# Kernel tuning notes

Hardware: AMD Instinct MI355X
Metric: run time of the kernel (lower is better)

The kernel has to match this reference:

```python
import jax, jax.numpy as jnp
import numpy as np

N_NODES = 50000
N_EDGES = 600000
N_GRAPHS = 1000
IN_DIM = 128   # atom_feat_dim
HID = 128      # emb_dim
NEG_SLOPE = 0.01


def setup_inputs() -> dict:
    key = jax.random.key(0)
    k = jax.random.split(key, 6)
    drug_x = jax.random.normal(k[0], (N_NODES, IN_DIM), dtype=jnp.float32)
    edge_index = jax.random.randint(k[1], (2, N_EDGES), 0, N_NODES, dtype=jnp.int32)
    batch = jnp.sort(jax.random.randint(k[2], (N_NODES,), 0, N_GRAPHS, dtype=jnp.int32))
    # GCNConv parameters (glorot-ish init for weights, zero bias, as in PyG)
    W1 = jax.random.normal(k[3], (IN_DIM, HID), dtype=jnp.float32) * (1.0 / np.sqrt(IN_DIM))
    b1 = jnp.zeros((HID,), dtype=jnp.float32)
    W2 = jax.random.normal(k[4], (HID, HID), dtype=jnp.float32) * (1.0 / np.sqrt(HID))
    b2 = jnp.zeros((HID,), dtype=jnp.float32)
    return {"drug_x": drug_x, "W1": W1, "b1": b1, "W2": W2, "b2": b2,
            "edge_index": edge_index, "batch": batch}


def _gcn_conv(x, W, b, src, dst, n_nodes):
    """PyG GCNConv: lin -> add self-loops -> deg^-1/2 sym norm -> scatter-add -> +bias."""
    h = x @ W  # [N, H]
    ones = jnp.ones(src.shape[0], dtype=h.dtype)
    # degree on the target side, +1 for the self-loop
    deg = jax.ops.segment_sum(ones, dst, num_segments=n_nodes) + 1.0
    dinv = jax.lax.rsqrt(deg)  # [N]
    coef = dinv[src] * dinv[dst]  # [E]
    agg = jax.ops.segment_sum(h[src] * coef[:, None], dst, num_segments=n_nodes)
    # self-loop contribution: dinv[i]*dinv[i]*h[i]
    agg = agg + h * (dinv * dinv)[:, None]
    return agg + b


def _leaky_relu(x):
    return jnp.where(x > 0, x, NEG_SLOPE * x)


def reference(drug_x, W1, b1, W2, b2, edge_index, batch):
    src, dst = edge_index[0], edge_index[1]
    n = drug_x.shape[0]
    h = _leaky_relu(_gcn_conv(drug_x, W1, b1, src, dst, n))  # dropout = identity (eval)
    h = _leaky_relu(_gcn_conv(h, W2, b2, src, dst, n))
    # global_mean_pool over graph ids
    sums = jax.ops.segment_sum(h, batch, num_segments=N_GRAPHS)
    counts = jax.ops.segment_sum(jnp.ones((n,), h.dtype), batch, num_segments=N_GRAPHS)
    return sums / jnp.maximum(counts, 1.0)[:, None]
```

## Files before the change

### kernel.cpp

```cpp
#include <hip/hip_runtime.h>

#define DIM 128
#define NEG_SLOPE 0.01f
#define ELLW 64
#define CPAD 16
#define LDA 136
#define SPLIT 4
#define WPAD 132

typedef short short8 __attribute__((ext_vector_type(8)));
typedef float f32x4 __attribute__((ext_vector_type(4)));

__device__ __forceinline__ unsigned short f2bf(float f) {
    unsigned u = __float_as_uint(f);
    u = u + 0x7FFFu + ((u >> 16) & 1u);
    return (unsigned short)(u >> 16);
}
__device__ __forceinline__ float bf2f(unsigned short s) {
    return __uint_as_float((unsigned)s << 16);
}

__global__ __launch_bounds__(256) void k_fillprep(const int* __restrict__ src,
                                                  const int* __restrict__ dst,
                                                  const int* __restrict__ batch,
                                                  int* __restrict__ cursorPad,
                                                  int* __restrict__ eSrc,
                                                  const float* __restrict__ W1,
                                                  const float* __restrict__ W2,
                                                  unsigned short* __restrict__ Wt1,
                                                  unsigned short* __restrict__ Wt2,
                                                  int* __restrict__ gOff,
                                                  int nE, int nN, int nG) {
    int i = blockIdx.x * 256 + threadIdx.x;
    if (i < nE) {
        int s = src[i], d = dst[i];
        int pos = atomicAdd(&cursorPad[d * CPAD], 1);
        if (pos < ELLW) eSrc[(size_t)d * ELLW + pos] = s;
    }
    if (i < nN) {
        int b1 = batch[i];
        int b0 = (i == 0) ? -1 : batch[i - 1];
        for (int g = b0 + 1; g <= b1; ++g) gOff[g] = i;
        if (i == nN - 1) {
            for (int g = b1 + 1; g <= nG; ++g) gOff[g] = nN;
        }
    }
    if (i < 32768) {
        const float* W = (i < 16384) ? W1 : W2;
        unsigned short* Wt = (i < 16384) ? Wt1 : Wt2;
        int j = i & 16383;
        int k = j >> 7, n = j & 127;
        Wt[n * 128 + k] = f2bf(W[k * 128 + n]);
    }
}

__global__ __launch_bounds__(256) void k_gemm(const float* __restrict__ X,
                                              const unsigned short* __restrict__ Wt,
                                              const int* __restrict__ cursorPad,
                                              unsigned short* __restrict__ Y, int nRows) {
    __shared__ unsigned short sA[64 * LDA];
    const int t = threadIdx.x;
    const int row0 = blockIdx.x * 64;

#pragma unroll
    for (int rep = 0; rep < 8; ++rep) {
        int idx = t + rep * 256;
        int r = idx >> 5, k4 = (idx & 31) * 4;
        int gr = row0 + r;
        float4 v = make_float4(0.f, 0.f, 0.f, 0.f);
        if (gr < nRows) v = *(const float4*)&X[(size_t)gr * 128 + k4];
        ushort4 p;
        p.x = f2bf(v.x); p.y = f2bf(v.y); p.z = f2bf(v.z); p.w = f2bf(v.w);
        *(ushort4*)&sA[r * LDA + k4] = p;
    }
    __syncthreads();

    const int wave = t >> 6, lane = t & 63;
    const int l15 = lane & 15;
    const int koff = (lane >> 4) * 8;
    const int arow = wave * 16 + l15;

    short8 a[4];
#pragma unroll
    for (int ks = 0; ks < 4; ++ks)
        a[ks] = *(const short8*)&sA[arow * LDA + ks * 32 + koff];

    f32x4 acc[8];
#pragma unroll
    for (int c = 0; c < 8; ++c) acc[c] = (f32x4){0.f, 0.f, 0.f, 0.f};
#pragma unroll
    for (int c = 0; c < 8; ++c) {
        const unsigned short* wp = Wt + (size_t)(c * 16 + l15) * 128 + koff;
#pragma unroll
        for (int ks = 0; ks < 4; ++ks) {
            short8 b = *(const short8*)(wp + ks * 32);
            acc[c] = __builtin_amdgcn_mfma_f32_16x16x32_bf16(a[ks], b, acc[c], 0, 0, 0);
        }
    }
    const int orow = row0 + wave * 16 + (lane >> 4) * 4;
#pragma unroll
    for (int r = 0; r < 4; ++r) {
        int gr = orow + r;
        if (gr < nRows) {
            float dv = rsqrtf((float)cursorPad[gr * CPAD] + 1.0f);
#pragma unroll
            for (int c = 0; c < 8; ++c)
                Y[(size_t)gr * 128 + c * 16 + l15] = f2bf(acc[c][r] * dv);
        }
    }
}

#define ACCUM(v)                                         \
    do {                                                 \
        acc[0] += bf2f((v).x & 0xFFFFu);                 \
        acc[1] += __uint_as_float((v).x & 0xFFFF0000u);  \
        acc[2] += bf2f((v).y & 0xFFFFu);                 \
        acc[3] += __uint_as_float((v).y & 0xFFFF0000u);  \
        acc[4] += bf2f((v).z & 0xFFFFu);                 \
        acc[5] += __uint_as_float((v).z & 0xFFFF0000u);  \
        acc[6] += bf2f((v).w & 0xFFFFu);                 \
        acc[7] += __uint_as_float((v).w & 0xFFFF0000u);  \
    } while (0)

#define ACCUMF(v, s)                                                      \
    do {                                                                  \
        acc[0] = fmaf(bf2f((v).x & 0xFFFFu), (s), acc[0]);                \
        acc[1] = fmaf(__uint_as_float((v).x & 0xFFFF0000u), (s), acc[1]); \
        acc[2] = fmaf(bf2f((v).y & 0xFFFFu), (s), acc[2]);                \
        acc[3] = fmaf(__uint_as_float((v).y & 0xFFFF0000u), (s), acc[3]); \
        acc[4] = fmaf(bf2f((v).z & 0xFFFFu), (s), acc[4]);                \
        acc[5] = fmaf(__uint_as_float((v).z & 0xFFFF0000u), (s), acc[5]); \
        acc[6] = fmaf(bf2f((v).w & 0xFFFFu), (s), acc[6]);                \
        acc[7] = fmaf(__uint_as_float((v).w & 0xFFFF0000u), (s), acc[7]); \
    } while (0)

__device__ __forceinline__ void gather_body(const uint4* __restrict__ h4,
                                            const int* __restrict__ cursorPad,
                                            const int* __restrict__ eSrc,
                                            const float* __restrict__ bias,
                                            int i, int l, float* acc, int nN) {
    const int beg = i * ELLW;

    int4 s0 = *(const int4*)&eSrc[beg];
    int4 s1 = *(const int4*)&eSrc[beg + 4];
    int4 s2 = *(const int4*)&eSrc[beg + 8];
    int4 s3 = *(const int4*)&eSrc[beg + 12];
    const int cnt = cursorPad[i * CPAD];
    const uint4 hv = h4[(size_t)i * 16 + l];

    int sidx[16];
    sidx[0]  = s0.x; sidx[1]  = s0.y; sidx[2]  = s0.z; sidx[3]  = s0.w;
    sidx[4]  = s1.x; sidx[5]  = s1.y; sidx[6]  = s1.z; sidx[7]  = s1.w;
    sidx[8]  = s2.x; sidx[9]  = s2.y; sidx[10] = s2.z; sidx[11] = s2.w;
    sidx[12] = s3.x; sidx[13] = s3.y; sidx[14] = s3.z; sidx[15] = s3.w;
#pragma unroll
    for (int j = 0; j < 16; ++j) {
        unsigned us = (unsigned)sidx[j];
        sidx[j] = (us < (unsigned)nN) ? sidx[j] : 0;
    }

    uint4 v[16];
#pragma unroll
    for (int j = 0; j < 16; ++j) v[j] = h4[(size_t)sidx[j] * 16 + l];

    const int deg = min(cnt, ELLW);
    const int end = beg + deg;
    const float di = rsqrtf((float)cnt + 1.0f);

    acc[0] = bf2f(hv.x & 0xFFFFu);
    acc[1] = __uint_as_float(hv.x & 0xFFFF0000u);
    acc[2] = bf2f(hv.y & 0xFFFFu);
    acc[3] = __uint_as_float(hv.y & 0xFFFF0000u);
    acc[4] = bf2f(hv.z & 0xFFFFu);
    acc[5] = __uint_as_float(hv.z & 0xFFFF0000u);
    acc[6] = bf2f(hv.w & 0xFFFFu);
    acc[7] = __uint_as_float(hv.w & 0xFFFF0000u);

#pragma unroll
    for (int j = 0; j < 16; ++j) {
        float sc = (j < deg) ? 1.0f : 0.0f;
        ACCUMF(v[j], sc);
    }

    int e = beg + 16;
    for (; e + 8 <= end; e += 8) {
        int4 t0 = *(const int4*)&eSrc[e];
        int4 t1 = *(const int4*)&eSrc[e + 4];
        uint4 w[8];
        w[0] = h4[(size_t)t0.x * 16 + l];
        w[1] = h4[(size_t)t0.y * 16 + l];
        w[2] = h4[(size_t)t0.z * 16 + l];
        w[3] = h4[(size_t)t0.w * 16 + l];
        w[4] = h4[(size_t)t1.x * 16 + l];
        w[5] = h4[(size_t)t1.y * 16 + l];
        w[6] = h4[(size_t)t1.z * 16 + l];
        w[7] = h4[(size_t)t1.w * 16 + l];
#pragma unroll
        for (int j = 0; j < 8; ++j) ACCUM(w[j]);
    }
    if (e + 4 <= end) {
        int4 t0 = *(const int4*)&eSrc[e];
        uint4 w[4];
        w[0] = h4[(size_t)t0.x * 16 + l];
        w[1] = h4[(size_t)t0.y * 16 + l];
        w[2] = h4[(size_t)t0.z * 16 + l];
        w[3] = h4[(size_t)t0.w * 16 + l];
#pragma unroll
        for (int j = 0; j < 4; ++j) ACCUM(w[j]);
        e += 4;
    }
    if (e + 2 <= end) {
        int t0 = eSrc[e], t1 = eSrc[e + 1];
        uint4 w0 = h4[(size_t)t0 * 16 + l];
        uint4 w1 = h4[(size_t)t1 * 16 + l];
        ACCUM(w0);
        ACCUM(w1);
        e += 2;
    }
    if (e < end) {
        int t0 = eSrc[e];
        uint4 w0 = h4[(size_t)t0 * 16 + l];
        ACCUM(w0);
    }

    float4 b0 = *(const float4*)&bias[l * 8];
    float4 b1 = *(const float4*)&bias[l * 8 + 4];
    acc[0] = acc[0] * di + b0.x; acc[0] = acc[0] > 0.f ? acc[0] : NEG_SLOPE * acc[0];
    acc[1] = acc[1] * di + b0.y; acc[1] = acc[1] > 0.f ? acc[1] : NEG_SLOPE * acc[1];
    acc[2] = acc[2] * di + b0.z; acc[2] = acc[2] > 0.f ? acc[2] : NEG_SLOPE * acc[2];
    acc[3] = acc[3] * di + b0.w; acc[3] = acc[3] > 0.f ? acc[3] : NEG_SLOPE * acc[3];
    acc[4] = acc[4] * di + b1.x; acc[4] = acc[4] > 0.f ? acc[4] : NEG_SLOPE * acc[4];
    acc[5] = acc[5] * di + b1.y; acc[5] = acc[5] > 0.f ? acc[5] : NEG_SLOPE * acc[5];
    acc[6] = acc[6] * di + b1.z; acc[6] = acc[6] > 0.f ? acc[6] : NEG_SLOPE * acc[6];
    acc[7] = acc[7] * di + b1.w; acc[7] = acc[7] > 0.f ? acc[7] : NEG_SLOPE * acc[7];
}
#undef ACCUM
#undef ACCUMF

__global__ __launch_bounds__(256) void k_gg(const uint4* __restrict__ h4in,
                                            const int* __restrict__ cursorPad,
                                            const int* __restrict__ eSrc,
                                            const float* __restrict__ bias,
                                            const unsigned short* __restrict__ Wt,
                                            unsigned short* __restrict__ Y, int nN) {
    __shared__ unsigned short sA[16 * LDA];
    const int t = threadIdx.x;
    const int row0 = blockIdx.x * 16;
    const int lg = t >> 4;
    const int l = t & 15;

    {
        int i = row0 + lg;
        float acc[8];
        if (i < nN) {
            gather_body(h4in, cursorPad, eSrc, bias, i, l, acc, nN);
        } else {
#pragma unroll
            for (int j = 0; j < 8; ++j) acc[j] = 0.0f;
        }
        ushort4 p0, p1;
        p0.x = f2bf(acc[0]); p0.y = f2bf(acc[1]); p0.z = f2bf(acc[2]); p0.w = f2bf(acc[3]);
        p1.x = f2bf(acc[4]); p1.y = f2bf(acc[5]); p1.z = f2bf(acc[6]); p1.w = f2bf(acc[7]);
        *(ushort4*)&sA[lg * LDA + l * 8] = p0;
        *(ushort4*)&sA[lg * LDA + l * 8 + 4] = p1;
    }
    __syncthreads();

    const int wave = t >> 6, lane = t & 63;
    const int l15 = lane & 15;
    const int koff = (lane >> 4) * 8;

    short8 a[4];
#pragma unroll
    for (int ks = 0; ks < 4; ++ks)
        a[ks] = *(const short8*)&sA[l15 * LDA + ks * 32 + koff];

    f32x4 acc[2];
#pragma unroll
    for (int cb = 0; cb < 2; ++cb) acc[cb] = (f32x4){0.f, 0.f, 0.f, 0.f};
#pragma unroll
    for (int cb = 0; cb < 2; ++cb) {
        const int c = wave * 2 + cb;
        const unsigned short* wp = Wt + (size_t)(c * 16 + l15) * 128 + koff;
#pragma unroll
        for (int ks = 0; ks < 4; ++ks) {
            short8 b = *(const short8*)(wp + ks * 32);
            acc[cb] = __builtin_amdgcn_mfma_f32_16x16x32_bf16(a[ks], b, acc[cb], 0, 0, 0);
        }
    }
    const int orow = row0 + (lane >> 4) * 4;
#pragma unroll
    for (int r = 0; r < 4; ++r) {
        int gr = orow + r;
        if (gr < nN) {
            float dv = rsqrtf((float)cursorPad[gr * CPAD] + 1.0f);
#pragma unroll
            for (int cb = 0; cb < 2; ++cb)
                Y[(size_t)gr * 128 + (wave * 2 + cb) * 16 + l15] = f2bf(acc[cb][r] * dv);
        }
    }
}

__global__ __launch_bounds__(256) void k_gp(const uint4* __restrict__ h4in,
                                            const int* __restrict__ cursorPad,
                                            const int* __restrict__ eSrc,
                                            const float* __restrict__ bias,
                                            const int* __restrict__ gOff,
                                            float* __restrict__ out, int nN, int nG) {
    __shared__ float accW[4 * WPAD];
    const int g = blockIdx.x / SPLIT;
    const int part = blockIdx.x % SPLIT;
    const int t = threadIdx.x;
    const int beg = gOff[g], end = gOff[g + 1];
    const int lg = t >> 4, l = t & 15;
    const int wave = t >> 6, lane = t & 63;

    float acc8[8];
#pragma unroll
    for (int j = 0; j < 8; ++j) acc8[j] = 0.0f;

    for (int base = beg + part * 16; base < end; base += SPLIT * 16) {
        int i = base + lg;
        if (i < end) {
            float a[8];
            gather_body(h4in, cursorPad, eSrc, bias, i, l, a, nN);
#pragma unroll
            for (int j = 0; j < 8; ++j) acc8[j] += a[j];
        }
    }
#pragma unroll
    for (int j = 0; j < 8; ++j) {
        acc8[j] += __shfl_down(acc8[j], 32);
        acc8[j] += __shfl_down(acc8[j], 16);
    }
    if (lane < 16) {
        *(float4*)&accW[wave * WPAD + lane * 8] =
            make_float4(acc8[0], acc8[1], acc8[2], acc8[3]);
        *(float4*)&accW[wave * WPAD + lane * 8 + 4] =
            make_float4(acc8[4], acc8[5], acc8[6], acc8[7]);
    }
    __syncthreads();
    if (t < 128) {
        float s = accW[0 * WPAD + t] + accW[1 * WPAD + t] +
                  accW[2 * WPAD + t] + accW[3 * WPAD + t];
        float cnt = (float)(end - beg);
        atomicAdd(&out[(size_t)g * DIM + t], s / fmaxf(cnt, 1.0f));
    }
}

extern "C" void kernel_launch(void* const* d_in, const int* in_sizes, int n_in,
                              void* d_out, int out_size, void* d_ws, size_t ws_size,
                              hipStream_t stream) {
    const float* X  = (const float*)d_in[0];
    const float* W1 = (const float*)d_in[1];
    const float* b1 = (const float*)d_in[2];
    const float* W2 = (const float*)d_in[3];
    const float* b2 = (const float*)d_in[4];
    const int*   ei = (const int*)d_in[5];
    const int*   batch = (const int*)d_in[6];
    float* out = (float*)d_out;

    const int NN = in_sizes[0] / DIM;
    const int NE = in_sizes[5] / 2;
    const int NG = out_size / DIM;

    const int* src = ei;
    const int* dst = ei + NE;

    char* ws = (char*)d_ws;
    size_t o = 0;
    auto alloc = [&](size_t bytes) {
        char* p = ws + o;
        o += (bytes + 1023) & ~(size_t)1023;
        return p;
    };
    int* cursorPad = (int*)alloc((size_t)NN * CPAD * 4);
    int* gOff      = (int*)alloc((size_t)(NG + 1) * 4);
    unsigned short* Wt1 = (unsigned short*)alloc((size_t)16384 * 2);
    unsigned short* Wt2 = (unsigned short*)alloc((size_t)16384 * 2);
    int*   eSrc    = (int*)alloc((size_t)NN * ELLW * 4);
    unsigned short* bufA = (unsigned short*)alloc((size_t)NN * DIM * 2);
    unsigned short* bufB = (unsigned short*)alloc((size_t)NN * DIM * 2);

    hipMemsetAsync(cursorPad, 0, (size_t)NN * CPAD * 4, stream);
    hipMemsetAsync(out, 0, (size_t)out_size * 4, stream);

    const int B = 256;

    k_fillprep<<<(NE + B - 1) / B, B, 0, stream>>>(src, dst, batch, cursorPad, eSrc,
                                                   W1, W2, Wt1, Wt2, gOff, NE, NN, NG);

    k_gemm<<<(NN + 63) / 64, B, 0, stream>>>(X, Wt1, cursorPad, bufA, NN);

    k_gg<<<(NN + 15) / 16, B, 0, stream>>>((const uint4*)bufA, cursorPad, eSrc, b1,
                                           Wt2, bufB, NN);

    k_gp<<<NG * SPLIT, B, 0, stream>>>((const uint4*)bufB, cursorPad, eSrc, b2,
                                       gOff, out, NN, NG);
}
```

Before: 196.3 us.

## Chunk features into 32-column slabs and pack neighbor lists with 16-bit indices

Stores intermediate bf16 features in four column-chunked slabs so each gather block touches a smaller working set that fits in cache better. Packs the degree and the first 30 neighbor indices as 16-bit values into one 64-byte metadata row per node, with overflow going to a 16-bit ELL array. The fused gather+GEMM kernel is split into separate gather and GEMM2 kernels, and pooling now writes its output directly instead of using atomics. Nontemporal loads and stores are added throughout. The 16-bit indices only work while the node count stays below 65536, and unused index slots are read as zero-filled entries, which relies on the memset.

Result: slower. 225.4 us (+14.8%).

```diff
diff --git a/kernel.cpp b/kernel.cpp
--- a/kernel.cpp
+++ b/kernel.cpp
@@ -2,14 +2,16 @@
 
 #define DIM 128
 #define NEG_SLOPE 0.01f
+#define NCHUNK 4
+#define CH 32
 #define ELLW 64
-#define CPAD 16
+#define MIDX 30
 #define LDA 136
-#define SPLIT 4
-#define WPAD 132
 
 typedef short short8 __attribute__((ext_vector_type(8)));
 typedef float f32x4 __attribute__((ext_vector_type(4)));
+typedef unsigned int u32x4 __attribute__((ext_vector_type(4)));
+typedef unsigned short ushort_t;
 
 __device__ __forceinline__ unsigned short f2bf(float f) {
     unsigned u = __float_as_uint(f);
@@ -23,8 +25,9 @@
 __global__ __launch_bounds__(256) void k_fillprep(const int* __restrict__ src,
                                                   const int* __restrict__ dst,
                                                   const int* __restrict__ batch,
-                                                  int* __restrict__ cursorPad,
-                                                  int* __restrict__ eSrc,
+                                                  unsigned int* __restrict__ metaU,
+                                                  unsigned short* __restrict__ metaH,
+                                                  unsigned short* __restrict__ eSrcU,
                                                   const float* __restrict__ W1,
                                                   const float* __restrict__ W2,
                                                   unsigned short* __restrict__ Wt1,
@@ -34,8 +37,9 @@
     int i = blockIdx.x * 256 + threadIdx.x;
     if (i < nE) {
         int s = src[i], d = dst[i];
-        int pos = atomicAdd(&cursorPad[d * CPAD], 1);
-        if (pos < ELLW) eSrc[(size_t)d * ELLW + pos] = s;
+        int pos = atomicAdd((int*)&metaU[(size_t)d * 16], 1);
+        if (pos < MIDX) metaH[(size_t)d * 32 + 2 + pos] = (unsigned short)s;
+        else if (pos < ELLW) eSrcU[(size_t)d * ELLW + pos] = (unsigned short)s;
     }
     if (i < nN) {
         int b1 = batch[i];
@@ -51,62 +55,6 @@
         int j = i & 16383;
         int k = j >> 7, n = j & 127;
         Wt[n * 128 + k] = f2bf(W[k * 128 + n]);
-    }
-}
-
-__global__ __launch_bounds__(256) void k_gemm(const float* __restrict__ X,
-                                              const unsigned short* __restrict__ Wt,
-                                              const int* __restrict__ cursorPad,
-                                              unsigned short* __restrict__ Y, int nRows) {
-    __shared__ unsigned short sA[64 * LDA];
-    const int t = threadIdx.x;
-    const int row0 = blockIdx.x * 64;
-
-#pragma unroll
-    for (int rep = 0; rep < 8; ++rep) {
-        int idx = t + rep * 256;
-        int r = idx >> 5, k4 = (idx & 31) * 4;
-        int gr = row0 + r;
-        float4 v = make_float4(0.f, 0.f, 0.f, 0.f);
-        if (gr < nRows) v = *(const float4*)&X[(size_t)gr * 128 + k4];
-        ushort4 p;
-        p.x = f2bf(v.x); p.y = f2bf(v.y); p.z = f2bf(v.z); p.w = f2bf(v.w);
-        *(ushort4*)&sA[r * LDA + k4] = p;
-    }
-    __syncthreads();
-
-    const int wave = t >> 6, lane = t & 63;
-    const int l15 = lane & 15;
-    const int koff = (lane >> 4) * 8;
-    const int arow = wave * 16 + l15;
-
-    short8 a[4];
-#pragma unroll
-    for (int ks = 0; ks < 4; ++ks)
-        a[ks] = *(const short8*)&sA[arow * LDA + ks * 32 + koff];
-
-    f32x4 acc[8];
-#pragma unroll
-    for (int c = 0; c < 8; ++c) acc[c] = (f32x4){0.f, 0.f, 0.f, 0.f};
-#pragma unroll
-    for (int c = 0; c < 8; ++c) {
-        const unsigned short* wp = Wt + (size_t)(c * 16 + l15) * 128 + koff;
-#pragma unroll
-        for (int ks = 0; ks < 4; ++ks) {
-            short8 b = *(const short8*)(wp + ks * 32);
-            acc[c] = __builtin_amdgcn_mfma_f32_16x16x32_bf16(a[ks], b, acc[c], 0, 0, 0);
-        }
-    }
-    const int orow = row0 + wave * 16 + (lane >> 4) * 4;
-#pragma unroll
-    for (int r = 0; r < 4; ++r) {
-        int gr = orow + r;
-        if (gr < nRows) {
-            float dv = rsqrtf((float)cursorPad[gr * CPAD] + 1.0f);
-#pragma unroll
-            for (int c = 0; c < 8; ++c)
-                Y[(size_t)gr * 128 + c * 16 + l15] = f2bf(acc[c][r] * dv);
-        }
     }
 }
 
@@ -127,6 +75,18 @@
         acc[0] = fmaf(bf2f((v).x & 0xFFFFu), (s), acc[0]);                \
         acc[1] = fmaf(__uint_as_float((v).x & 0xFFFF0000u), (s), acc[1]); \
         acc[2] = fmaf(bf2f((v).y & 0xFFFFu), (s), acc[2]);                \
+        acc[3] = fmaf(bf2f((v).y >> 16 << 16 == 0 ? 0 : (unsigned short)((v).y >> 16)) * 0.f + __uint_as_float((v).y & 0xFFFF0000u), (s), acc[3]); \
+        acc[4] = fmaf(bf2f((v).z & 0xFFFFu), (s), acc[4]);                \
+        acc[5] = fmaf(__uint_as_float((v).z & 0xFFFF0000u), (s), acc[5]); \
+        acc[6] = fmaf(bf2f((v).w & 0xFFFFu), (s), acc[6]);                \
+        acc[7] = fmaf(__uint_as_float((v).w & 0xFFFF0000u), (s), acc[7]); \
+    } while (0)
+#undef ACCUMF
+#define ACCUMF(v, s)                                                      \
+    do {                                                                  \
+        acc[0] = fmaf(bf2f((v).x & 0xFFFFu), (s), acc[0]);                \
+        acc[1] = fmaf(__uint_as_float((v).x & 0xFFFF0000u), (s), acc[1]); \
+        acc[2] = fmaf(bf2f((v).y & 0xFFFFu), (s), acc[2]);                \
         acc[3] = fmaf(__uint_as_float((v).y & 0xFFFF0000u), (s), acc[3]); \
         acc[4] = fmaf(bf2f((v).z & 0xFFFFu), (s), acc[4]);                \
         acc[5] = fmaf(__uint_as_float((v).z & 0xFFFF0000u), (s), acc[5]); \
@@ -134,37 +94,41 @@
         acc[7] = fmaf(__uint_as_float((v).w & 0xFFFF0000u), (s), acc[7]); \
     } while (0)
 
-__device__ __forceinline__ void gather_body(const uint4* __restrict__ h4,
-                                            const int* __restrict__ cursorPad,
-                                            const int* __restrict__ eSrc,
-                                            const float* __restrict__ bias,
-                                            int i, int l, float* acc, int nN) {
-    const int beg = i * ELLW;
-
-    int4 s0 = *(const int4*)&eSrc[beg];
-    int4 s1 = *(const int4*)&eSrc[beg + 4];
-    int4 s2 = *(const int4*)&eSrc[beg + 8];
-    int4 s3 = *(const int4*)&eSrc[beg + 12];
-    const int cnt = cursorPad[i * CPAD];
-    const uint4 hv = h4[(size_t)i * 16 + l];
-
-    int sidx[16];
-    sidx[0]  = s0.x; sidx[1]  = s0.y; sidx[2]  = s0.z; sidx[3]  = s0.w;
-    sidx[4]  = s1.x; sidx[5]  = s1.y; sidx[6]  = s1.z; sidx[7]  = s1.w;
-    sidx[8]  = s2.x; sidx[9]  = s2.y; sidx[10] = s2.z; sidx[11] = s2.w;
-    sidx[12] = s3.x; sidx[13] = s3.y; sidx[14] = s3.z; sidx[15] = s3.w;
-#pragma unroll
-    for (int j = 0; j < 16; ++j) {
-        unsigned us = (unsigned)sidx[j];
-        sidx[j] = (us < (unsigned)nN) ? sidx[j] : 0;
-    }
-
-    uint4 v[16];
-#pragma unroll
-    for (int j = 0; j < 16; ++j) v[j] = h4[(size_t)sidx[j] * 16 + l];
+__device__ __forceinline__ void gather_chunk(const u32x4* __restrict__ hb,
+                                             const u32x4* __restrict__ meta4,
+                                             const unsigned short* __restrict__ eSrcU,
+                                             const float* __restrict__ bias,
+                                             int i, int l, float* acc) {
+    const u32x4* mrow = meta4 + (size_t)i * 4;
+    u32x4 m0 = __builtin_nontemporal_load(mrow + 0);
+    u32x4 m1 = __builtin_nontemporal_load(mrow + 1);
+    u32x4 m2 = __builtin_nontemporal_load(mrow + 2);
+    u32x4 m3 = __builtin_nontemporal_load(mrow + 3);
+    u32x4 hv = hb[(size_t)i * 4 + l];
+
+    const int cnt = (int)m0.x;
+    int idx[30];
+    idx[0]  = m0.y & 0xFFFFu;  idx[1]  = m0.y >> 16;
+    idx[2]  = m0.z & 0xFFFFu;  idx[3]  = m0.z >> 16;
+    idx[4]  = m0.w & 0xFFFFu;  idx[5]  = m0.w >> 16;
+    idx[6]  = m1.x & 0xFFFFu;  idx[7]  = m1.x >> 16;
+    idx[8]  = m1.y & 0xFFFFu;  idx[9]  = m1.y >> 16;
+    idx[10] = m1.z & 0xFFFFu;  idx[11] = m1.z >> 16;
+    idx[12] = m1.w & 0xFFFFu;  idx[13] = m1.w >> 16;
+    idx[14] = m2.x & 0xFFFFu;  idx[15] = m2.x >> 16;
+    idx[16] = m2.y & 0xFFFFu;  idx[17] = m2.y >> 16;
+    idx[18] = m2.z & 0xFFFFu;  idx[19] = m2.z >> 16;
+    idx[20] = m2.w & 0xFFFFu;  idx[21] = m2.w >> 16;
+    idx[22] = m3.x & 0xFFFFu;  idx[23] = m3.x >> 16;
+    idx[24] = m3.y & 0xFFFFu;  idx[25] = m3.y >> 16;
+    idx[26] = m3.z & 0xFFFFu;  idx[27] = m3.z >> 16;
+    idx[28] = m3.w & 0xFFFFu;  idx[29] = m3.w >> 16;
+
+    u32x4 v[16];
+#pragma unroll
+    for (int j = 0; j < 16; ++j) v[j] = hb[(size_t)idx[j] * 4 + l];
 
     const int deg = min(cnt, ELLW);
-    const int end = beg + deg;
     const float di = rsqrtf((float)cnt + 1.0f);
 
     acc[0] = bf2f(hv.x & 0xFFFFu);
@@ -182,45 +146,23 @@
         ACCUMF(v[j], sc);
     }
 
-    int e = beg + 16;
-    for (; e + 8 <= end; e += 8) {
-        int4 t0 = *(const int4*)&eSrc[e];
-        int4 t1 = *(const int4*)&eSrc[e + 4];
-        uint4 w[8];
-        w[0] = h4[(size_t)t0.x * 16 + l];
-        w[1] = h4[(size_t)t0.y * 16 + l];
-        w[2] = h4[(size_t)t0.z * 16 + l];
-        w[3] = h4[(size_t)t0.w * 16 + l];
-        w[4] = h4[(size_t)t1.x * 16 + l];
-        w[5] = h4[(size_t)t1.y * 16 + l];
-        w[6] = h4[(size_t)t1.z * 16 + l];
-        w[7] = h4[(size_t)t1.w * 16 + l];
-#pragma unroll
-        for (int j = 0; j < 8; ++j) ACCUM(w[j]);
-    }
-    if (e + 4 <= end) {
-        int4 t0 = *(const int4*)&eSrc[e];
-        uint4 w[4];
-        w[0] = h4[(size_t)t0.x * 16 + l];
-        w[1] = h4[(size_t)t0.y * 16 + l];
-        w[2] = h4[(size_t)t0.z * 16 + l];
-        w[3] = h4[(size_t)t0.w * 16 + l];
-#pragma unroll
-        for (int j = 0; j < 4; ++j) ACCUM(w[j]);
-        e += 4;
-    }
-    if (e + 2 <= end) {
-        int t0 = eSrc[e], t1 = eSrc[e + 1];
-        uint4 w0 = h4[(size_t)t0 * 16 + l];
-        uint4 w1 = h4[(size_t)t1 * 16 + l];
-        ACCUM(w0);
-        ACCUM(w1);
-        e += 2;
-    }
-    if (e < end) {
-        int t0 = eSrc[e];
-        uint4 w0 = h4[(size_t)t0 * 16 + l];
-        ACCUM(w0);
+    if (deg > 16) {
+        u32x4 w[14];
+#pragma unroll
+        for (int j = 0; j < 14; ++j) w[j] = hb[(size_t)idx[16 + j] * 4 + l];
+#pragma unroll
+        for (int j = 0; j < 14; ++j) {
+            float sc = (16 + j < deg) ? 1.0f : 0.0f;
+            ACCUMF(w[j], sc);
+        }
+    }
+
+    if (deg > MIDX) {
+        for (int e = MIDX; e < deg; ++e) {
+            int s = (int)__builtin_nontemporal_load(&eSrcU[(size_t)i * ELLW + e]);
+            u32x4 w0 = hb[(size_t)s * 4 + l];
+            ACCUM(w0);
+        }
     }
 
     float4 b0 = *(const float4*)&bias[l * 8];
@@ -234,96 +176,177 @@
     acc[6] = acc[6] * di + b1.z; acc[6] = acc[6] > 0.f ? acc[6] : NEG_SLOPE * acc[6];
     acc[7] = acc[7] * di + b1.w; acc[7] = acc[7] > 0.f ? acc[7] : NEG_SLOPE * acc[7];
 }
-#undef ACCUM
-#undef ACCUMF
-
-__global__ __launch_bounds__(256) void k_gg(const uint4* __restrict__ h4in,
-                                            const int* __restrict__ cursorPad,
-                                            const int* __restrict__ eSrc,
-                                            const float* __restrict__ bias,
-                                            const unsigned short* __restrict__ Wt,
-                                            unsigned short* __restrict__ Y, int nN) {
-    __shared__ unsigned short sA[16 * LDA];
+
+__global__ __launch_bounds__(256) void k_gemm1(const float* __restrict__ X,
+                                               const unsigned short* __restrict__ Wt,
+                                               const unsigned int* __restrict__ metaU,
+                                               unsigned short* __restrict__ Y, int nRows) {
+    __shared__ unsigned short sA[64 * LDA];
     const int t = threadIdx.x;
-    const int row0 = blockIdx.x * 16;
-    const int lg = t >> 4;
-    const int l = t & 15;
-
-    {
-        int i = row0 + lg;
-        float acc[8];
-        if (i < nN) {
-            gather_body(h4in, cursorPad, eSrc, bias, i, l, acc, nN);
-        } else {
-#pragma unroll
-            for (int j = 0; j < 8; ++j) acc[j] = 0.0f;
-        }
-        ushort4 p0, p1;
-        p0.x = f2bf(acc[0]); p0.y = f2bf(acc[1]); p0.z = f2bf(acc[2]); p0.w = f2bf(acc[3]);
-        p1.x = f2bf(acc[4]); p1.y = f2bf(acc[5]); p1.z = f2bf(acc[6]); p1.w = f2bf(acc[7]);
-        *(ushort4*)&sA[lg * LDA + l * 8] = p0;
-        *(ushort4*)&sA[lg * LDA + l * 8 + 4] = p1;
+    const int row0 = blockIdx.x * 64;
+
+#pragma unroll
+    for (int rep = 0; rep < 8; ++rep) {
+        int idx = t + rep * 256;
+        int r = idx >> 5, k4 = (idx & 31) * 4;
+        int gr = row0 + r;
+        f32x4 v = (f32x4){0.f, 0.f, 0.f, 0.f};
+        if (gr < nRows) v = __builtin_nontemporal_load((const f32x4*)&X[(size_t)gr * 128 + k4]);
+        ushort4 p;
+        p.x = f2bf(v.x); p.y = f2bf(v.y); p.z = f2bf(v.z); p.w = f2bf(v.w);
+        *(ushort4*)&sA[r * LDA + k4] = p;
     }
     __syncthreads();
 
     const int wave = t >> 6, lane = t & 63;
     const int l15 = lane & 15;
     const int koff = (lane >> 4) * 8;
+    const int arow = wave * 16 + l15;
 
     short8 a[4];
 #pragma unroll
     for (int ks = 0; ks < 4; ++ks)
-        a[ks] = *(const short8*)&sA[l15 * LDA + ks * 32 + koff];
-
-    f32x4 acc[2];
-#pragma unroll
-    for (int cb = 0; cb < 2; ++cb) acc[cb] = (f32x4){0.f, 0.f, 0.f, 0.f};
-#pragma unroll
-    for (int cb = 0; cb < 2; ++cb) {
-        const int c = wave * 2 + cb;
+        a[ks] = *(const short8*)&sA[arow * LDA + ks * 32 + koff];
+
+    f32x4 acc[8];
+#pragma unroll
+    for (int c = 0; c < 8; ++c) acc[c] = (f32x4){0.f, 0.f, 0.f, 0.f};
+#pragma unroll
+    for (int c = 0; c < 8; ++c) {
         const unsigned short* wp = Wt + (size_t)(c * 16 + l15) * 128 + koff;
 #pragma unroll
         for (int ks = 0; ks < 4; ++ks) {
             short8 b = *(const short8*)(wp + ks * 32);
-            acc[cb] = __builtin_amdgcn_mfma_f32_16x16x32_bf16(a[ks], b, acc[cb], 0, 0, 0);
-        }
-    }
-    const int orow = row0 + (lane >> 4) * 4;
+            acc[c] = __builtin_amdgcn_mfma_f32_16x16x32_bf16(a[ks], b, acc[c], 0, 0, 0);
+        }
+    }
+    const int orow = row0 + wave * 16 + (lane >> 4) * 4;
 #pragma unroll
     for (int r = 0; r < 4; ++r) {
         int gr = orow + r;
-        if (gr < nN) {
-            float dv = rsqrtf((float)cursorPad[gr * CPAD] + 1.0f);
-#pragma unroll
-            for (int cb = 0; cb < 2; ++cb)
-                Y[(size_t)gr * 128 + (wave * 2 + cb) * 16 + l15] = f2bf(acc[cb][r] * dv);
-        }
-    }
-}
-
-__global__ __launch_bounds__(256) void k_gp(const uint4* __restrict__ h4in,
-                                            const int* __restrict__ cursorPad,
-                                            const int* __restrict__ eSrc,
+        if (gr < nRows) {
+            int cnt = (int)__builtin_nontemporal_load(&metaU[(size_t)gr * 16]);
+            float dv = rsqrtf((float)cnt + 1.0f);
+#pragma unroll
+            for (int c = 0; c < 8; ++c) {
+                size_t addr = ((size_t)((c >> 1) * nRows) + gr) * CH + (c & 1) * 16 + l15;
+                __builtin_nontemporal_store(f2bf(acc[c][r] * dv), &Y[addr]);
+            }
+        }
+    }
+}
+
+__global__ __launch_bounds__(256) void k_gemm2(const unsigned short* __restrict__ Xb,
+                                               const unsigned short* __restrict__ Wt,
+                                               const unsigned int* __restrict__ metaU,
+                                               unsigned short* __restrict__ Y, int nRows) {
+    __shared__ unsigned short sA[64 * LDA];
+    const int t = threadIdx.x;
+    const int row0 = blockIdx.x * 64;
+
+#pragma unroll
+    for (int rep = 0; rep < 4; ++rep) {
+        int idx = t + rep * 256;
+        int r = idx >> 4, s = idx & 15;
+        int c = s >> 2, q = s & 3;
+        int gr = row0 + r;
+        u32x4 v = (u32x4){0u, 0u, 0u, 0u};
+        if (gr < nRows)
+            v = __builtin_nontemporal_load(
+                (const u32x4*)&Xb[((size_t)(c * nRows) + gr) * CH + q * 8]);
+        *(u32x4*)&sA[r * LDA + s * 8] = v;
+    }
+    __syncthreads();
+
+    const int wave = t >> 6, lane = t & 63;
+    const int l15 = lane & 15;
+    const int koff = (lane >> 4) * 8;
+    const int arow = wave * 16 + l15;
+
+    short8 a[4];
+#pragma unroll
+    for (int ks = 0; ks < 4; ++ks)
+        a[ks] = *(const short8*)&sA[arow * LDA + ks * 32 + koff];
+
+    f32x4 acc[8];
+#pragma unroll
+    for (int c = 0; c < 8; ++c) acc[c] = (f32x4){0.f, 0.f, 0.f, 0.f};
+#pragma unroll
+    for (int c = 0; c < 8; ++c) {
+        const unsigned short* wp = Wt + (size_t)(c * 16 + l15) * 128 + koff;
+#pragma unroll
+        for (int ks = 0; ks < 4; ++ks) {
+            short8 b = *(const short8*)(wp + ks * 32);
+            acc[c] = __builtin_amdgcn_mfma_f32_16x16x32_bf16(a[ks], b, acc[c], 0, 0, 0);
+        }
+    }
+    const int orow = row0 + wave * 16 + (lane >> 4) * 4;
+#pragma unroll
+    for (int r = 0; r < 4; ++r) {
+        int gr = orow + r;
+        if (gr < nRows) {
+            int cnt = (int)__builtin_nontemporal_load(&metaU[(size_t)gr * 16]);
+            float dv = rsqrtf((float)cnt + 1.0f);
+#pragma unroll
+            for (int c = 0; c < 8; ++c) {
+                size_t addr = ((size_t)((c >> 1) * nRows) + gr) * CH + (c & 1) * 16 + l15;
+                __builtin_nontemporal_store(f2bf(acc[c][r] * dv), &Y[addr]);
+            }
+        }
+    }
+}
+
+__global__ __launch_bounds__(256) void k_gather1(const u32x4* __restrict__ hbase,
+                                                 const u32x4* __restrict__ meta4,
+                                                 const unsigned short* __restrict__ eSrcU,
+                                                 const float* __restrict__ bias,
+                                                 unsigned short* __restrict__ outB,
+                                                 int nN) {
+    const int tile = blockIdx.x >> 2;
+    const int c = blockIdx.x & 3;
+    const int t = threadIdx.x;
+    const int i = tile * 64 + (t >> 2);
+    const int l = t & 3;
+    if (i >= nN) return;
+
+    const u32x4* hb = hbase + (size_t)c * nN * 4;
+    float acc[8];
+    gather_chunk(hb, meta4, eSrcU, bias + c * CH, i, l, acc);
+
+    u32x4 p;
+    p.x = (unsigned)f2bf(acc[0]) | ((unsigned)f2bf(acc[1]) << 16);
+    p.y = (unsigned)f2bf(acc[2]) | ((unsigned)f2bf(acc[3]) << 16);
+    p.z = (unsigned)f2bf(acc[4]) | ((unsigned)f2bf(acc[5]) << 16);
+    p.w = (unsigned)f2bf(acc[6]) | ((unsigned)f2bf(acc[7]) << 16);
+    __builtin_nontemporal_store(
+        p, (u32x4*)&outB[((size_t)(c * nN) + i) * CH + l * 8]);
+}
+
+__global__ __launch_bounds__(256) void k_gp(const u32x4* __restrict__ hbase,
+                                            const u32x4* __restrict__ meta4,
+                                            const unsigned short* __restrict__ eSrcU,
                                             const float* __restrict__ bias,
                                             const int* __restrict__ gOff,
-                                            float* __restrict__ out, int nN, int nG) {
-    __shared__ float accW[4 * WPAD];
-    const int g = blockIdx.x / SPLIT;
-    const int part = blockIdx.x % SPLIT;
+                                            float* __restrict__ out, int nN) {
+    __shared__ float red[4 * 32];
+    const int g = blockIdx.x >> 2;
+    const int c = blockIdx.x & 3;
     const int t = threadIdx.x;
     const int beg = gOff[g], end = gOff[g + 1];
-    const int lg = t >> 4, l = t & 15;
+    const int ln = t >> 2, l = t & 3;
     const int wave = t >> 6, lane = t & 63;
 
+    const u32x4* hb = hbase + (size_t)c * nN * 4;
+
     float acc8[8];
 #pragma unroll
     for (int j = 0; j < 8; ++j) acc8[j] = 0.0f;
 
-    for (int base = beg + part * 16; base < end; base += SPLIT * 16) {
-        int i = base + lg;
+    for (int i0 = beg; i0 < end; i0 += 64) {
+        int i = i0 + ln;
         if (i < end) {
             float a[8];
-            gather_body(h4in, cursorPad, eSrc, bias, i, l, a, nN);
+            gather_chunk(hb, meta4, eSrcU, bias + c * CH, i, l, a);
 #pragma unroll
             for (int j = 0; j < 8; ++j) acc8[j] += a[j];
         }
@@ -332,19 +355,18 @@
     for (int j = 0; j < 8; ++j) {
         acc8[j] += __shfl_down(acc8[j], 32);
         acc8[j] += __shfl_down(acc8[j], 16);
-    }
-    if (lane < 16) {
-        *(float4*)&accW[wave * WPAD + lane * 8] =
-            make_float4(acc8[0], acc8[1], acc8[2], acc8[3]);
-        *(float4*)&accW[wave * WPAD + lane * 8 + 4] =
-            make_float4(acc8[4], acc8[5], acc8[6], acc8[7]);
+        acc8[j] += __shfl_down(acc8[j], 8);
+        acc8[j] += __shfl_down(acc8[j], 4);
+    }
+    if (lane < 4) {
+#pragma unroll
+        for (int j = 0; j < 8; ++j) red[wave * 32 + lane * 8 + j] = acc8[j];
     }
     __syncthreads();
-    if (t < 128) {
-        float s = accW[0 * WPAD + t] + accW[1 * WPAD + t] +
-                  accW[2 * WPAD + t] + accW[3 * WPAD + t];
-        float cnt = (float)(end - beg);
-        atomicAdd(&out[(size_t)g * DIM + t], s / fmaxf(cnt, 1.0f));
+    if (t < 32) {
+        float s = red[t] + red[32 + t] + red[64 + t] + red[96 + t];
+        float n = (float)(end - beg);
+        out[(size_t)g * DIM + c * CH + t] = s / fmaxf(n, 1.0f);
     }
 }
 
@@ -374,27 +396,31 @@
         o += (bytes + 1023) & ~(size_t)1023;
         return p;
     };
-    int* cursorPad = (int*)alloc((size_t)NN * CPAD * 4);
-    int* gOff      = (int*)alloc((size_t)(NG + 1) * 4);
+    unsigned int* meta = (unsigned int*)alloc((size_t)NN * 64);
+    int* gOff          = (int*)alloc((size_t)(NG + 1) * 4);
     unsigned short* Wt1 = (unsigned short*)alloc((size_t)16384 * 2);
     unsigned short* Wt2 = (unsigned short*)alloc((size_t)16384 * 2);
-    int*   eSrc    = (int*)alloc((size_t)NN * ELLW * 4);
+    unsigned short* eSrcU = (unsigned short*)alloc((size_t)NN * ELLW * 2);
     unsigned short* bufA = (unsigned short*)alloc((size_t)NN * DIM * 2);
     unsigned short* bufB = (unsigned short*)alloc((size_t)NN * DIM * 2);
-
-    hipMemsetAsync(cursorPad, 0, (size_t)NN * CPAD * 4, stream);
-    hipMemsetAsync(out, 0, (size_t)out_size * 4, stream);
+    unsigned short* bufC = (unsigned short*)alloc((size_t)NN * DIM * 2);
+
+    hipMemsetAsync(meta, 0, (size_t)NN * 64, stream);
 
     const int B = 256;
-
-    k_fillprep<<<(NE + B - 1) / B, B, 0, stream>>>(src, dst, batch, cursorPad, eSrc,
+    const int nT = (NN + 63) / 64;
+
+    k_fillprep<<<(NE + B - 1) / B, B, 0, stream>>>(src, dst, batch, meta,
+                                                   (unsigned short*)meta, eSrcU,
                                                    W1, W2, Wt1, Wt2, gOff, NE, NN, NG);
 
-    k_gemm<<<(NN + 63) / 64, B, 0, stream>>>(X, Wt1, cursorPad, bufA, NN);
-
-    k_gg<<<(NN + 15) / 16, B, 0, stream>>>((const uint4*)bufA, cursorPad, eSrc, b1,
-                                           Wt2, bufB, NN);
-
-    k_gp<<<NG * SPLIT, B, 0, stream>>>((const uint4*)bufB, cursorPad, eSrc, b2,
-                                       gOff, out, NN, NG);
-}
+    k_gemm1<<<nT, B, 0, stream>>>(X, Wt1, meta, bufA, NN);
+
+    k_gather1<<<nT * NCHUNK, B, 0, stream>>>((const u32x4*)bufA, (const u32x4*)meta,
+                                             eSrcU, b1, bufB, NN);
+
+    k_gemm2<<<nT, B, 0, stream>>>(bufB, Wt2, meta, bufC, NN);
+
+    k_gp<<<NG * NCHUNK, B, 0, stream>>>((const u32x4*)bufC, (const u32x4*)meta,
+                                        eSrcU, b2, gOff, out, NN);
+}
```

## Pack degree and 16-bit neighbor indices into one 64-byte row per node

Applied to the files above, without the earlier changes.

Replaces the padded cursor array and the 64-wide int32 ELL table with a compact per-node 64-byte metadata row holding the count plus 30 uint16 source indices, and a uint16 spill area for neighbors 31 to 64. The gather then reads the count and first 30 indices in four uint4 loads, and the memset and index traffic shrink. Nontemporal loads and stores are added on the edge, X and output streams. This relies on node ids fitting in 16 bits, which holds only for N=50000, and it drops the bounds clamp on indices.

New measurement: 206.0 us. 1.05x slower.

```diff
diff --git a/kernel.cpp b/kernel.cpp
--- a/kernel.cpp
+++ b/kernel.cpp
@@ -2,8 +2,9 @@
 
 #define DIM 128
 #define NEG_SLOPE 0.01f
-#define ELLW 64
-#define CPAD 16
+#define MIDX 30
+#define SPILLW 34
+#define CAP 64
 #define LDA 136
 #define SPLIT 4
 #define WPAD 132
@@ -23,8 +24,9 @@
 __global__ __launch_bounds__(256) void k_fillprep(const int* __restrict__ src,
                                                   const int* __restrict__ dst,
                                                   const int* __restrict__ batch,
-                                                  int* __restrict__ cursorPad,
-                                                  int* __restrict__ eSrc,
+                                                  unsigned int* __restrict__ metaU,
+                                                  unsigned short* __restrict__ metaH,
+                                                  unsigned short* __restrict__ spill,
                                                   const float* __restrict__ W1,
                                                   const float* __restrict__ W2,
                                                   unsigned short* __restrict__ Wt1,
@@ -33,9 +35,11 @@
                                                   int nE, int nN, int nG) {
     int i = blockIdx.x * 256 + threadIdx.x;
     if (i < nE) {
-        int s = src[i], d = dst[i];
-        int pos = atomicAdd(&cursorPad[d * CPAD], 1);
-        if (pos < ELLW) eSrc[(size_t)d * ELLW + pos] = s;
+        int s = __builtin_nontemporal_load(&src[i]);
+        int d = __builtin_nontemporal_load(&dst[i]);
+        int pos = atomicAdd((int*)&metaU[(size_t)d * 16], 1);
+        if (pos < MIDX) metaH[(size_t)d * 32 + 2 + pos] = (unsigned short)s;
+        else if (pos < CAP) spill[(size_t)d * SPILLW + (pos - MIDX)] = (unsigned short)s;
     }
     if (i < nN) {
         int b1 = batch[i];
@@ -51,62 +55,6 @@
         int j = i & 16383;
         int k = j >> 7, n = j & 127;
         Wt[n * 128 + k] = f2bf(W[k * 128 + n]);
-    }
-}
-
-__global__ __launch_bounds__(256) void k_gemm(const float* __restrict__ X,
-                                              const unsigned short* __restrict__ Wt,
-                                              const int* __restrict__ cursorPad,
-                                              unsigned short* __restrict__ Y, int nRows) {
-    __shared__ unsigned short sA[64 * LDA];
-    const int t = threadIdx.x;
-    const int row0 = blockIdx.x * 64;
-
-#pragma unroll
-    for (int rep = 0; rep < 8; ++rep) {
-        int idx = t + rep * 256;
-        int r = idx >> 5, k4 = (idx & 31) * 4;
-        int gr = row0 + r;
-        float4 v = make_float4(0.f, 0.f, 0.f, 0.f);
-        if (gr < nRows) v = *(const float4*)&X[(size_t)gr * 128 + k4];
-        ushort4 p;
-        p.x = f2bf(v.x); p.y = f2bf(v.y); p.z = f2bf(v.z); p.w = f2bf(v.w);
-        *(ushort4*)&sA[r * LDA + k4] = p;
-    }
-    __syncthreads();
-
-    const int wave = t >> 6, lane = t & 63;
-    const int l15 = lane & 15;
-    const int koff = (lane >> 4) * 8;
-    const int arow = wave * 16 + l15;
-
-    short8 a[4];
-#pragma unroll
-    for (int ks = 0; ks < 4; ++ks)
-        a[ks] = *(const short8*)&sA[arow * LDA + ks * 32 + koff];
-
-    f32x4 acc[8];
-#pragma unroll
-    for (int c = 0; c < 8; ++c) acc[c] = (f32x4){0.f, 0.f, 0.f, 0.f};
-#pragma unroll
-    for (int c = 0; c < 8; ++c) {
-        const unsigned short* wp = Wt + (size_t)(c * 16 + l15) * 128 + koff;
-#pragma unroll
-        for (int ks = 0; ks < 4; ++ks) {
-            short8 b = *(const short8*)(wp + ks * 32);
-            acc[c] = __builtin_amdgcn_mfma_f32_16x16x32_bf16(a[ks], b, acc[c], 0, 0, 0);
-        }
-    }
-    const int orow = row0 + wave * 16 + (lane >> 4) * 4;
-#pragma unroll
-    for (int r = 0; r < 4; ++r) {
-        int gr = orow + r;
-        if (gr < nRows) {
-            float dv = rsqrtf((float)cursorPad[gr * CPAD] + 1.0f);
-#pragma unroll
-            for (int c = 0; c < 8; ++c)
-                Y[(size_t)gr * 128 + c * 16 + l15] = f2bf(acc[c][r] * dv);
-        }
     }
 }
 
@@ -135,37 +83,34 @@
     } while (0)
 
 __device__ __forceinline__ void gather_body(const uint4* __restrict__ h4,
-                                            const int* __restrict__ cursorPad,
-                                            const int* __restrict__ eSrc,
+                                            const uint4* __restrict__ meta4,
+                                            const unsigned short* __restrict__ spill,
                                             const float* __restrict__ bias,
-                                            int i, int l, float* acc, int nN) {
-    const int beg = i * ELLW;
-
-    int4 s0 = *(const int4*)&eSrc[beg];
-    int4 s1 = *(const int4*)&eSrc[beg + 4];
-    int4 s2 = *(const int4*)&eSrc[beg + 8];
-    int4 s3 = *(const int4*)&eSrc[beg + 12];
-    const int cnt = cursorPad[i * CPAD];
+                                            int i, int l, float* acc) {
+    const uint4* mrow = meta4 + (size_t)i * 4;
+    uint4 m0 = mrow[0];
+    uint4 m1 = mrow[1];
+    uint4 m2 = mrow[2];
+    uint4 m3 = mrow[3];
     const uint4 hv = h4[(size_t)i * 16 + l];
 
-    int sidx[16];
-    sidx[0]  = s0.x; sidx[1]  = s0.y; sidx[2]  = s0.z; sidx[3]  = s0.w;
-    sidx[4]  = s1.x; sidx[5]  = s1.y; sidx[6]  = s1.z; sidx[7]  = s1.w;
-    sidx[8]  = s2.x; sidx[9]  = s2.y; sidx[10] = s2.z; sidx[11] = s2.w;
-    sidx[12] = s3.x; sidx[13] = s3.y; sidx[14] = s3.z; sidx[15] = s3.w;
-#pragma unroll
-    for (int j = 0; j < 16; ++j) {
-        unsigned us = (unsigned)sidx[j];
-        sidx[j] = (us < (unsigned)nN) ? sidx[j] : 0;
-    }
+    const int cnt = (int)m0.x;
+    const int deg = min(cnt, CAP);
+    const float di = rsqrtf((float)cnt + 1.0f);
+
+    int idx[16];
+    idx[0]  = m0.y & 0xFFFFu;  idx[1]  = m0.y >> 16;
+    idx[2]  = m0.z & 0xFFFFu;  idx[3]  = m0.z >> 16;
+    idx[4]  = m0.w & 0xFFFFu;  idx[5]  = m0.w >> 16;
+    idx[6]  = m1.x & 0xFFFFu;  idx[7]  = m1.x >> 16;
+    idx[8]  = m1.y & 0xFFFFu;  idx[9]  = m1.y >> 16;
+    idx[10] = m1.z & 0xFFFFu;  idx[11] = m1.z >> 16;
+    idx[12] = m1.w & 0xFFFFu;  idx[13] = m1.w >> 16;
+    idx[14] = m2.x & 0xFFFFu;  idx[15] = m2.x >> 16;
 
     uint4 v[16];
 #pragma unroll
-    for (int j = 0; j < 16; ++j) v[j] = h4[(size_t)sidx[j] * 16 + l];
-
-    const int deg = min(cnt, ELLW);
-    const int end = beg + deg;
-    const float di = rsqrtf((float)cnt + 1.0f);
+    for (int j = 0; j < 16; ++j) v[j] = h4[(size_t)idx[j] * 16 + l];
 
     acc[0] = bf2f(hv.x & 0xFFFFu);
     acc[1] = __uint_as_float(hv.x & 0xFFFF0000u);
@@ -182,45 +127,31 @@
         ACCUMF(v[j], sc);
     }
 
-    int e = beg + 16;
-    for (; e + 8 <= end; e += 8) {
-        int4 t0 = *(const int4*)&eSrc[e];
-        int4 t1 = *(const int4*)&eSrc[e + 4];
-        uint4 w[8];
-        w[0] = h4[(size_t)t0.x * 16 + l];
-        w[1] = h4[(size_t)t0.y * 16 + l];
-        w[2] = h4[(size_t)t0.z * 16 + l];
-        w[3] = h4[(size_t)t0.w * 16 + l];
-        w[4] = h4[(size_t)t1.x * 16 + l];
-        w[5] = h4[(size_t)t1.y * 16 + l];
-        w[6] = h4[(size_t)t1.z * 16 + l];
-        w[7] = h4[(size_t)t1.w * 16 + l];
-#pragma unroll
-        for (int j = 0; j < 8; ++j) ACCUM(w[j]);
-    }
-    if (e + 4 <= end) {
-        int4 t0 = *(const int4*)&eSrc[e];
-        uint4 w[4];
-        w[0] = h4[(size_t)t0.x * 16 + l];
-        w[1] = h4[(size_t)t0.y * 16 + l];
-        w[2] = h4[(size_t)t0.z * 16 + l];
-        w[3] = h4[(size_t)t0.w * 16 + l];
-#pragma unroll
-        for (int j = 0; j < 4; ++j) ACCUM(w[j]);
-        e += 4;
-    }
-    if (e + 2 <= end) {
-        int t0 = eSrc[e], t1 = eSrc[e + 1];
-        uint4 w0 = h4[(size_t)t0 * 16 + l];
-        uint4 w1 = h4[(size_t)t1 * 16 + l];
-        ACCUM(w0);
-        ACCUM(w1);
-        e += 2;
-    }
-    if (e < end) {
-        int t0 = eSrc[e];
-        uint4 w0 = h4[(size_t)t0 * 16 + l];
-        ACCUM(w0);
+    if (deg > 16) {
+        int idx2[14];
+        idx2[0]  = m2.y & 0xFFFFu;  idx2[1]  = m2.y >> 16;
+        idx2[2]  = m2.z & 0xFFFFu;  idx2[3]  = m2.z >> 16;
+        idx2[4]  = m2.w & 0xFFFFu;  idx2[5]  = m2.w >> 16;
+        idx2[6]  = m3.x & 0xFFFFu;  idx2[7]  = m3.x >> 16;
+        idx2[8]  = m3.y & 0xFFFFu;  idx2[9]  = m3.y >> 16;
+        idx2[10] = m3.z & 0xFFFFu;  idx2[11] = m3.z >> 16;
+        idx2[12] = m3.w & 0xFFFFu;  idx2[13] = m3.w >> 16;
+        uint4 w[14];
+#pragma unroll
+        for (int j = 0; j < 14; ++j) w[j] = h4[(size_t)idx2[j] * 16 + l];
+#pragma unroll
+        for (int j = 0; j < 14; ++j) {
+            float sc = (16 + j < deg) ? 1.0f : 0.0f;
+            ACCUMF(w[j], sc);
+        }
+    }
+
+    if (deg > MIDX) {
+        for (int e = MIDX; e < deg; ++e) {
+            int s = (int)spill[(size_t)i * SPILLW + (e - MIDX)];
+            uint4 w0 = h4[(size_t)s * 16 + l];
+            ACCUM(w0);
+        }
     }
 
     float4 b0 = *(const float4*)&bias[l * 8];
@@ -234,12 +165,70 @@
     acc[6] = acc[6] * di + b1.z; acc[6] = acc[6] > 0.f ? acc[6] : NEG_SLOPE * acc[6];
     acc[7] = acc[7] * di + b1.w; acc[7] = acc[7] > 0.f ? acc[7] : NEG_SLOPE * acc[7];
 }
-#undef ACCUM
-#undef ACCUMF
+
+__global__ __launch_bounds__(256) void k_gemm(const float* __restrict__ X,
+                                              const unsigned short* __restrict__ Wt,
+                                              const unsigned int* __restrict__ metaU,
+                                              unsigned short* __restrict__ Y, int nRows) {
+    __shared__ unsigned short sA[64 * LDA];
+    const int t = threadIdx.x;
+    const int row0 = blockIdx.x * 64;
+
+#pragma unroll
+    for (int rep = 0; rep < 8; ++rep) {
+        int idx = t + rep * 256;
+        int r = idx >> 5, k4 = (idx & 31) * 4;
+        int gr = row0 + r;
+        f32x4 v = (f32x4){0.f, 0.f, 0.f, 0.f};
+        if (gr < nRows)
+            v = __builtin_nontemporal_load((const f32x4*)&X[(size_t)gr * 128 + k4]);
+        ushort4 p;
+        p.x = f2bf(v.x); p.y = f2bf(v.y); p.z = f2bf(v.z); p.w = f2bf(v.w);
+        *(ushort4*)&sA[r * LDA + k4] = p;
+    }
+    __syncthreads();
+
+    const int wave = t >> 6, lane = t & 63;
+    const int l15 = lane & 15;
+    const int koff = (lane >> 4) * 8;
+    const int arow = wave * 16 + l15;
+
+    short8 a[4];
+#pragma unroll
+    for (int ks = 0; ks < 4; ++ks)
+        a[ks] = *(const short8*)&sA[arow * LDA + ks * 32 + koff];
+
+    f32x4 acc[8];
+#pragma unroll
+    for (int c = 0; c < 8; ++c) acc[c] = (f32x4){0.f, 0.f, 0.f, 0.f};
+#pragma unroll
+    for (int c = 0; c < 8; ++c) {
+        const unsigned short* wp = Wt + (size_t)(c * 16 + l15) * 128 + koff;
+#pragma unroll
+        for (int ks = 0; ks < 4; ++ks) {
+            short8 b = *(const short8*)(wp + ks * 32);
+            acc[c] = __builtin_amdgcn_mfma_f32_16x16x32_bf16(a[ks], b, acc[c], 0, 0, 0);
+        }
+    }
+    const int orow = row0 + wave * 16 + (lane >> 4) * 4;
+#pragma unroll
+    for (int r = 0; r < 4; ++r) {
+        int gr = orow + r;
+        if (gr < nRows) {
+            int cnt = (int)metaU[(size_t)gr * 16];
+            float dv = rsqrtf((float)cnt + 1.0f);
+#pragma unroll
+            for (int c = 0; c < 8; ++c)
+                __builtin_nontemporal_store(f2bf(acc[c][r] * dv),
+                                            &Y[(size_t)gr * 128 + c * 16 + l15]);
+        }
+    }
+}
 
 __global__ __launch_bounds__(256) void k_gg(const uint4* __restrict__ h4in,
-                                            const int* __restrict__ cursorPad,
-                                            const int* __restrict__ eSrc,
+                                            const uint4* __restrict__ meta4,
+                                            const unsigned int* __restrict__ metaU,
+                                            const unsigned short* __restrict__ spill,
                                             const float* __restrict__ bias,
                                             const unsigned short* __restrict__ Wt,
                                             unsigned short* __restrict__ Y, int nN) {
@@ -253,7 +242,7 @@
         int i = row0 + lg;
         float acc[8];
         if (i < nN) {
-            gather_body(h4in, cursorPad, eSrc, bias, i, l, acc, nN);
+            gather_body(h4in, meta4, spill, bias, i, l, acc);
         } else {
 #pragma unroll
             for (int j = 0; j < 8; ++j) acc[j] = 0.0f;
@@ -293,17 +282,20 @@
     for (int r = 0; r < 4; ++r) {
         int gr = orow + r;
         if (gr < nN) {
-            float dv = rsqrtf((float)cursorPad[gr * CPAD] + 1.0f);
+            int cnt = (int)metaU[(size_t)gr * 16];
+            float dv = rsqrtf((float)cnt + 1.0f);
 #pragma unroll
             for (int cb = 0; cb < 2; ++cb)
-                Y[(size_t)gr * 128 + (wave * 2 + cb) * 16 + l15] = f2bf(acc[cb][r] * dv);
+                __builtin_nontemporal_store(
+                    f2bf(acc[cb][r] * dv),
+                    &Y[(size_t)gr * 128 + (wave * 2 + cb) * 16 + l15]);
         }
     }
 }
 
 __global__ __launch_bounds__(256) void k_gp(const uint4* __restrict__ h4in,
-                                            const int* __restrict__ cursorPad,
-                                            const int* __restrict__ eSrc,
+                                            const uint4* __restrict__ meta4,
+                                            const unsigned short* __restrict__ spill,
                                             const float* __restrict__ bias,
                                             const int* __restrict__ gOff,
                                             float* __restrict__ out, int nN, int nG) {
@@ -323,7 +315,7 @@
         int i = base + lg;
         if (i < end) {
             float a[8];
-            gather_body(h4in, cursorPad, eSrc, bias, i, l, a, nN);
+            gather_body(h4in, meta4, spill, bias, i, l, a);
 #pragma unroll
             for (int j = 0; j < 8; ++j) acc8[j] += a[j];
         }
@@ -374,27 +366,28 @@
         o += (bytes + 1023) & ~(size_t)1023;
         return p;
     };
-    int* cursorPad = (int*)alloc((size_t)NN * CPAD * 4);
-    int* gOff      = (int*)alloc((size_t)(NG + 1) * 4);
+    unsigned int* meta = (unsigned int*)alloc((size_t)NN * 64);
+    int* gOff          = (int*)alloc((size_t)(NG + 1) * 4);
     unsigned short* Wt1 = (unsigned short*)alloc((size_t)16384 * 2);
     unsigned short* Wt2 = (unsigned short*)alloc((size_t)16384 * 2);
-    int*   eSrc    = (int*)alloc((size_t)NN * ELLW * 4);
+    unsigned short* spill = (unsigned short*)alloc((size_t)NN * SPILLW * 2);
     unsigned short* bufA = (unsigned short*)alloc((size_t)NN * DIM * 2);
     unsigned short* bufB = (unsigned short*)alloc((size_t)NN * DIM * 2);
 
-    hipMemsetAsync(cursorPad, 0, (size_t)NN * CPAD * 4, stream);
+    hipMemsetAsync(meta, 0, (size_t)NN * 64, stream);
     hipMemsetAsync(out, 0, (size_t)out_size * 4, stream);
 
     const int B = 256;
 
-    k_fillprep<<<(NE + B - 1) / B, B, 0, stream>>>(src, dst, batch, cursorPad, eSrc,
+    k_fillprep<<<(NE + B - 1) / B, B, 0, stream>>>(src, dst, batch, meta,
+                                                   (unsigned short*)meta, spill,
                                                    W1, W2, Wt1, Wt2, gOff, NE, NN, NG);
 
-    k_gemm<<<(NN + 63) / 64, B, 0, stream>>>(X, Wt1, cursorPad, bufA, NN);
-
-    k_gg<<<(NN + 15) / 16, B, 0, stream>>>((const uint4*)bufA, cursorPad, eSrc, b1,
-                                           Wt2, bufB, NN);
-
-    k_gp<<<NG * SPLIT, B, 0, stream>>>((const uint4*)bufB, cursorPad, eSrc, b2,
-                                       gOff, out, NN, NG);
-}
+    k_gemm<<<(NN + 63) / 64, B, 0, stream>>>(X, Wt1, meta, bufA, NN);
+
+    k_gg<<<(NN + 15) / 16, B, 0, stream>>>((const uint4*)bufA, (const uint4*)meta,
+                                           meta, spill, b1, Wt2, bufB, NN);
+
+    k_gp<<<NG * SPLIT, B, 0, stream>>>((const uint4*)bufB, (const uint4*)meta,
+                                       spill, b2, gOff, out, NN, NG);
+}
```
